# Kernel tuning notes

Hardware: AMD Instinct MI355X
Metric: run time of the kernel (lower is better)

Reference implementation:

```python
import jax, jax.numpy as jnp
import numpy as np

D_MODEL = 256
N_LEVELS = 4
N_HEADS = 4
N_POINTS = 8
D_FFN = 1024
SHAPES = [(100, 152), (50, 76), (25, 38), (13, 19)]  # (H, W) per level
BATCH = 2


def setup_inputs() -> dict:
    key = jax.random.key(0)
    ks = list(jax.random.split(key, 16))
    Len = sum(h * w for h, w in SHAPES)  # 20197
    s = 0.02

    def lin(k, fin, fout):
        k1, k2 = jax.random.split(k)
        return (jax.random.normal(k1, (fin, fout), jnp.float32) * s,
                jax.random.normal(k2, (fout,), jnp.float32) * s)

    W_off, b_off = lin(ks[0], D_MODEL, N_HEADS * N_LEVELS * N_POINTS * 2)
    W_attn, b_attn = lin(ks[1], D_MODEL, N_HEADS * N_LEVELS * N_POINTS)
    W_val, b_val = lin(ks[2], D_MODEL, D_MODEL)
    W_out, b_out = lin(ks[3], D_MODEL, D_MODEL)
    W1, b1 = lin(ks[4], D_MODEL, D_FFN)
    W2, b2 = lin(ks[5], D_FFN, D_MODEL)
    starts = np.concatenate([[0], np.cumsum([h * w for h, w in SHAPES])[:-1]])
    return {
        "src_feat": jax.random.normal(ks[6], (BATCH, Len, D_MODEL), jnp.float32),
        "reference_points": jax.random.uniform(ks[7], (BATCH, Len, N_LEVELS, 2), jnp.float32),
        "key_feat": jax.random.normal(ks[8], (BATCH, Len, D_MODEL), jnp.float32),
        "spatial_shapes": jnp.array(SHAPES, jnp.int32),
        "level_start_index": jnp.array(starts, jnp.int32),
        "W_off": W_off, "b_off": b_off, "W_attn": W_attn, "b_attn": b_attn,
        "W_val": W_val, "b_val": b_val, "W_out": W_out, "b_out": b_out,
        "W1": W1, "b1": b1, "W2": W2, "b2": b2,
        "g1": jnp.ones((D_MODEL,), jnp.float32), "be1": jnp.zeros((D_MODEL,), jnp.float32),
        "g2": jnp.ones((D_MODEL,), jnp.float32), "be2": jnp.zeros((D_MODEL,), jnp.float32),
    }


def _layernorm(x, g, b, eps=1e-5):
    mu = jnp.mean(x, -1, keepdims=True)
    var = jnp.mean(jnp.square(x - mu), -1, keepdims=True)
    return (x - mu) * jax.lax.rsqrt(var + eps) * g + b


def _bilinear(v, loc, H, W):
    # v: (N, M, H*W, D); loc: (N, M, Lq, P, 2) normalized [0,1]
    # Matches F.grid_sample(mode='bilinear', padding_mode='zeros', align_corners=False)
    x = loc[..., 0] * W - 0.5
    y = loc[..., 1] * H - 0.5
    x0 = jnp.floor(x)
    y0 = jnp.floor(y)
    wx = x - x0
    wy = y - y0
    N, M, Lq, P = x.shape
    out = None
    for dy in (0, 1):
        for dx in (0, 1):
            xi = x0 + dx
            yi = y0 + dy
            w = (wx if dx else 1.0 - wx) * (wy if dy else 1.0 - wy)
            valid = (xi >= 0) & (xi < W) & (yi >= 0) & (yi < H)
            idx = (jnp.clip(yi, 0, H - 1) * W + jnp.clip(xi, 0, W - 1)).astype(jnp.int32)
            g = jnp.take_along_axis(v, idx.reshape(N, M, Lq * P, 1), axis=2)
            g = g.reshape(N, M, Lq, P, -1) * (w * jnp.asarray(valid, v.dtype))[..., None]
            out = g if out is None else out + g
    return out  # (N, M, Lq, P, D)


def reference(src_feat, reference_points, key_feat, spatial_shapes, level_start_index,
              W_off, b_off, W_attn, b_attn, W_val, b_val, W_out, b_out,
              W1, b1, W2, b2, g1, be1, g2, be2):
    N, Lq, C = src_feat.shape
    M, L, P = N_HEADS, N_LEVELS, N_POINTS
    D = C // M
    shapes = np.asarray(spatial_shapes)  # static per-level (H, W)
    # --- MSDeformAttn ---
    value = (key_feat @ W_val + b_val).reshape(N, -1, M, D)
    off = (src_feat @ W_off + b_off).reshape(N, Lq, M, L, P, 2)
    attn = jax.nn.softmax((src_feat @ W_attn + b_attn).reshape(N, Lq, M, L * P), axis=-1)
    attn = attn.reshape(N, Lq, M, L, P)
    normalizer = jnp.stack([spatial_shapes[:, 1], spatial_shapes[:, 0]], -1).astype(src_feat.dtype)  # (L,2)=(W,H)
    loc = reference_points[:, :, None, :, None, :] + off / normalizer[None, None, None, :, None, :]
    out = jnp.zeros((N, M, Lq, D), src_feat.dtype)
    start = 0
    for l in range(L):
        H, W = int(shapes[l, 0]), int(shapes[l, 1])
        v = value[:, start:start + H * W].transpose(0, 2, 1, 3)  # (N,M,HW,D)
        samp = _bilinear(v, loc[:, :, :, l].transpose(0, 2, 1, 3, 4), H, W)  # (N,M,Lq,P,D)
        out = out + jnp.einsum('nmqpd,nqmp->nmqd', samp, attn[:, :, :, l])
        start += H * W
    out = out.transpose(0, 2, 1, 3).reshape(N, Lq, C)
    src2 = out @ W_out + b_out
    # --- residual + norm + FFN (light=False, dropout=0) ---
    x = _layernorm(src_feat + src2, g1, be1)
    ffn = jax.nn.relu(x @ W1 + b1) @ W2 + b2
    x = _layernorm(x + ffn, g2, be2)
    return (x, loc, attn)
```

## Files before the change

kernel.cpp:

```cpp
#include <hip/hip_runtime.h>
#include <hip/hip_bf16.h>

#define LQ 20197
#define NBATCH 2
#define MROWS 40394
#define MR256 ((size_t)MROWS * 256)

typedef __attribute__((ext_vector_type(8))) short bf16x8;
typedef __attribute__((ext_vector_type(4))) float f32x4;
typedef __attribute__((ext_vector_type(2))) float f32x2;

__device__ __forceinline__ unsigned short f2bf(float f) {
    unsigned u = __float_as_uint(f);
    return (unsigned short)((u + 0x7fff + ((u >> 16) & 1)) >> 16);
}
__device__ __forceinline__ float bf2f(unsigned short b) {
    return __uint_as_float((unsigned)b << 16);
}

__global__ __launch_bounds__(256) void prep_w_k(
    const float* __restrict__ Wv, const float* __restrict__ Wo,
    const float* __restrict__ Wa, const float* __restrict__ Wu,
    const float* __restrict__ W1, const float* __restrict__ W2,
    const float* __restrict__ ba,
    unsigned short* __restrict__ BTv, unsigned short* __restrict__ BTo,
    unsigned short* __restrict__ BTa, unsigned short* __restrict__ BTu,
    unsigned short* __restrict__ BT1, unsigned short* __restrict__ BT2,
    float* __restrict__ battn)
{
    const size_t id0 = (size_t)blockIdx.x * blockDim.x + threadIdx.x;
    const size_t stride = (size_t)gridDim.x * blockDim.x;
    for (size_t i = id0; i < 65536; i += stride) {
        const int n = (int)(i >> 8), k = (int)(i & 255);
        BTv[i] = f2bf(Wv[k * 256 + n]);
        BTo[i] = f2bf(Wo[k * 256 + n]);
        BTu[i] = f2bf(Wu[k * 256 + n]);
        BTa[i] = (n < 128) ? f2bf(Wa[k * 128 + n]) : (unsigned short)0;
    }
    for (size_t i = id0; i < 262144; i += stride) {
        const int n = (int)(i >> 8), k = (int)(i & 255);
        BT1[i] = f2bf(W1[(size_t)k * 1024 + n]);
        const int n2 = (int)(i >> 10), k2 = (int)(i & 1023);
        BT2[i] = f2bf(W2[(size_t)k2 * 256 + n2]);
    }
    if (id0 < 256) battn[id0] = (id0 < 128) ? ba[id0] : 0.f;
}

enum { EP_VAL = 0, EP_LOC = 1, EP_ATTN = 2, EP_LN = 3, EP_FFN1 = 4 };

template<int EP, bool AF32>
__global__ __launch_bounds__(256) void gemm_k(
    const void* __restrict__ Ap, const unsigned short* __restrict__ BT,
    const float* __restrict__ bias, const float* __restrict__ aux,
    const float* __restrict__ g, const float* __restrict__ be,
    void* outp, void* outp2)
{
    __shared__ __align__(16) unsigned short As[64 * 64];
    __shared__ __align__(16) unsigned short Bs[256 * 64];
    __shared__ float ps[64][4], pq[64][4];
    __shared__ float mu_s[64], rs_s[64];

    const int tid = threadIdx.x;
    const int l = tid & 63, w = tid >> 6;
    const int lc = l & 15, rg = l >> 4;
    const int rowBase = blockIdx.x * 64;
    const unsigned short* BTb = BT + (size_t)blockIdx.y * 65536;

    f32x4 acc[4][4] = {};

    for (int k0 = 0; k0 < 256; k0 += 64) {
        if (k0) __syncthreads();
        #pragma unroll
        for (int p = 0; p < 2; ++p) {
            const int idx = tid + p * 256;
            const int r = idx >> 3, s = idx & 7;
            const int row = rowBase + r;
            bf16x8 v = {};
            if (AF32) {
                if (row < MROWS) {
                    const float* A = (const float*)Ap;
                    const float4 v0 = *(const float4*)(A + (size_t)row * 256 + k0 + s * 8);
                    const float4 v1 = *(const float4*)(A + (size_t)row * 256 + k0 + s * 8 + 4);
                    v[0] = (short)f2bf(v0.x); v[1] = (short)f2bf(v0.y);
                    v[2] = (short)f2bf(v0.z); v[3] = (short)f2bf(v0.w);
                    v[4] = (short)f2bf(v1.x); v[5] = (short)f2bf(v1.y);
                    v[6] = (short)f2bf(v1.z); v[7] = (short)f2bf(v1.w);
                }
            } else {
                if (row < MROWS)
                    v = *(const bf16x8*)((const unsigned short*)Ap + (size_t)row * 256 + k0 + s * 8);
            }
            *(bf16x8*)&As[r * 64 + ((s ^ (r & 7)) << 3)] = v;
        }
        #pragma unroll
        for (int p = 0; p < 8; ++p) {
            const int idx = tid + p * 256;
            const int n = idx >> 3, s = idx & 7;
            bf16x8 v = *(const bf16x8*)(BTb + (size_t)n * 256 + k0 + s * 8);
            *(bf16x8*)&Bs[n * 64 + ((s ^ (n & 7)) << 3)] = v;
        }
        __syncthreads();
        #pragma unroll
        for (int kk = 0; kk < 2; ++kk) {
            bf16x8 aF[4], bF[4];
            const int sl = kk * 4 + rg;
            #pragma unroll
            for (int i = 0; i < 4; ++i) {
                const int r = i * 16 + lc;
                aF[i] = *(const bf16x8*)&As[r * 64 + ((sl ^ (r & 7)) << 3)];
            }
            #pragma unroll
            for (int j = 0; j < 4; ++j) {
                const int n = w * 64 + j * 16 + lc;
                bF[j] = *(const bf16x8*)&Bs[n * 64 + ((sl ^ (n & 7)) << 3)];
            }
            #pragma unroll
            for (int i = 0; i < 4; ++i)
                #pragma unroll
                for (int j = 0; j < 4; ++j)
                    acc[i][j] = __builtin_amdgcn_mfma_f32_16x16x32_bf16(aF[i], bF[j], acc[i][j], 0, 0, 0);
        }
    }

    if (EP == EP_VAL) {
        unsigned short* out = (unsigned short*)outp;
        #pragma unroll
        for (int i = 0; i < 4; ++i)
            #pragma unroll
            for (int r4 = 0; r4 < 4; ++r4) {
                const int row = rowBase + i * 16 + rg * 4 + r4;
                if (row >= MROWS) continue;
                #pragma unroll
                for (int j = 0; j < 4; ++j) {
                    const int col = w * 64 + j * 16 + lc;
                    out[(size_t)row * 256 + col] = f2bf(acc[i][j][r4] + bias[col]);
                }
            }
    } else if (EP == EP_FFN1) {
        unsigned short* h0 = (unsigned short*)outp;
        unsigned short* h1 = (unsigned short*)outp2;
        unsigned short* hb = (blockIdx.y < 2) ? h0 : h1;
        const int cbase = (blockIdx.y & 1) * 256;
        #pragma unroll
        for (int i = 0; i < 4; ++i)
            #pragma unroll
            for (int r4 = 0; r4 < 4; ++r4) {
                const int row = rowBase + i * 16 + rg * 4 + r4;
                if (row >= MROWS) continue;
                #pragma unroll
                for (int j = 0; j < 4; ++j) {
                    const int col = w * 64 + j * 16 + lc;
                    const float t = fmaxf(acc[i][j][r4] + bias[blockIdx.y * 256 + col], 0.f);
                    hb[(size_t)row * 512 + cbase + col] = f2bf(t);
                }
            }
    } else if (EP == EP_LOC) {
        float* out = (float*)outp;
        const float INV[8] = {1.f/152, 1.f/100, 1.f/76, 1.f/50, 1.f/38, 1.f/25, 1.f/19, 1.f/13};
        #pragma unroll
        for (int i = 0; i < 4; ++i)
            #pragma unroll
            for (int r4 = 0; r4 < 4; ++r4) {
                const int row = rowBase + i * 16 + rg * 4 + r4;
                if (row >= MROWS) continue;
                #pragma unroll
                for (int j = 0; j < 4; ++j) {
                    const int col = w * 64 + j * 16 + lc;
                    const int lvl = (col >> 4) & 3, xy = col & 1;
                    const float off = acc[i][j][r4] + bias[col];
                    const float ref = aux[(size_t)row * 8 + lvl * 2 + xy];
                    out[(size_t)row * 256 + col] = ref + off * INV[lvl * 2 + xy];
                }
            }
    } else if (EP == EP_ATTN) {
        if (w >= 2) return;
        float* out = (float*)outp;
        #pragma unroll
        for (int i = 0; i < 4; ++i)
            #pragma unroll
            for (int r4 = 0; r4 < 4; ++r4) {
                const int row = rowBase + i * 16 + rg * 4 + r4;
                float v[4];
                #pragma unroll
                for (int j = 0; j < 4; ++j) v[j] = acc[i][j][r4] + bias[w * 64 + j * 16 + lc];
                float mA = fmaxf(v[0], v[1]), mB = fmaxf(v[2], v[3]);
                #pragma unroll
                for (int o = 1; o <= 8; o <<= 1) {
                    mA = fmaxf(mA, __shfl_xor(mA, o));
                    mB = fmaxf(mB, __shfl_xor(mB, o));
                }
                float e[4];
                e[0] = __expf(v[0] - mA); e[1] = __expf(v[1] - mA);
                e[2] = __expf(v[2] - mB); e[3] = __expf(v[3] - mB);
                float sA = e[0] + e[1], sB = e[2] + e[3];
                #pragma unroll
                for (int o = 1; o <= 8; o <<= 1) {
                    sA += __shfl_xor(sA, o);
                    sB += __shfl_xor(sB, o);
                }
                if (row >= MROWS) continue;
                #pragma unroll
                for (int j = 0; j < 4; ++j) {
                    const int col = w * 64 + j * 16 + lc;
                    out[(size_t)row * 128 + col] = e[j] / (j < 2 ? sA : sB);
                }
            }
    } else {
        unsigned short* out = (unsigned short*)outp;
        #pragma unroll
        for (int i = 0; i < 4; ++i)
            #pragma unroll
            for (int r4 = 0; r4 < 4; ++r4) {
                const int row = rowBase + i * 16 + rg * 4 + r4;
                float s = 0.f, q = 0.f;
                #pragma unroll
                for (int j = 0; j < 4; ++j) {
                    const int col = w * 64 + j * 16 + lc;
                    float t = acc[i][j][r4] + bias[col];
                    if (row < MROWS) t += aux[(size_t)row * 256 + col];
                    acc[i][j][r4] = t;
                    s += t; q += t * t;
                }
                #pragma unroll
                for (int o = 1; o <= 8; o <<= 1) { s += __shfl_xor(s, o); q += __shfl_xor(q, o); }
                if (lc == 0) { ps[i * 16 + rg * 4 + r4][w] = s; pq[i * 16 + rg * 4 + r4][w] = q; }
            }
        __syncthreads();
        if (tid < 64) {
            const float s = ps[tid][0] + ps[tid][1] + ps[tid][2] + ps[tid][3];
            const float q = pq[tid][0] + pq[tid][1] + pq[tid][2] + pq[tid][3];
            const float m = s * (1.f / 256.f);
            mu_s[tid] = m;
            rs_s[tid] = rsqrtf(q * (1.f / 256.f) - m * m + 1e-5f);
        }
        __syncthreads();
        #pragma unroll
        for (int i = 0; i < 4; ++i)
            #pragma unroll
            for (int r4 = 0; r4 < 4; ++r4) {
                const int rl = i * 16 + rg * 4 + r4;
                const int row = rowBase + rl;
                if (row >= MROWS) continue;
                const float m = mu_s[rl], r = rs_s[rl];
                #pragma unroll
                for (int j = 0; j < 4; ++j) {
                    const int col = w * 64 + j * 16 + lc;
                    out[(size_t)row * 256 + col] = f2bf((acc[i][j][r4] - m) * r * g[col] + be[col]);
                }
            }
    }
}

__global__ __launch_bounds__(256) void ffn2_k(
    const unsigned short* __restrict__ h0, const unsigned short* __restrict__ h1,
    const unsigned short* __restrict__ BT2,
    const float* __restrict__ bias, const unsigned short* __restrict__ xb,
    const float* __restrict__ g, const float* __restrict__ be,
    float* __restrict__ out)
{
    __shared__ __align__(16) unsigned short As[64 * 64];
    __shared__ __align__(16) unsigned short Bs[256 * 64];
    __shared__ float ps[64][4], pq[64][4];
    __shared__ float mu_s[64], rs_s[64];

    const int tid = threadIdx.x;
    const int l = tid & 63, w = tid >> 6;
    const int lc = l & 15, rg = l >> 4;
    const int rowBase = blockIdx.x * 64;

    f32x4 acc[4][4] = {};

    for (int kc = 0; kc < 16; ++kc) {
        if (kc) __syncthreads();
        const unsigned short* Ab = (kc < 8) ? h0 : h1;
        const int koff = (kc & 7) * 64;
        #pragma unroll
        for (int p = 0; p < 2; ++p) {
            const int idx = tid + p * 256;
            const int r = idx >> 3, s = idx & 7;
            const int row = rowBase + r;
            bf16x8 v = {};
            if (row < MROWS) v = *(const bf16x8*)(Ab + (size_t)row * 512 + koff + s * 8);
            *(bf16x8*)&As[r * 64 + ((s ^ (r & 7)) << 3)] = v;
        }
        #pragma unroll
        for (int p = 0; p < 8; ++p) {
            const int idx = tid + p * 256;
            const int n = idx >> 3, s = idx & 7;
            bf16x8 v = *(const bf16x8*)(BT2 + (size_t)n * 1024 + kc * 64 + s * 8);
            *(bf16x8*)&Bs[n * 64 + ((s ^ (n & 7)) << 3)] = v;
        }
        __syncthreads();
        #pragma unroll
        for (int kk = 0; kk < 2; ++kk) {
            bf16x8 aF[4], bF[4];
            const int sl = kk * 4 + rg;
            #pragma unroll
            for (int i = 0; i < 4; ++i) {
                const int r = i * 16 + lc;
                aF[i] = *(const bf16x8*)&As[r * 64 + ((sl ^ (r & 7)) << 3)];
            }
            #pragma unroll
            for (int j = 0; j < 4; ++j) {
                const int n = w * 64 + j * 16 + lc;
                bF[j] = *(const bf16x8*)&Bs[n * 64 + ((sl ^ (n & 7)) << 3)];
            }
            #pragma unroll
            for (int i = 0; i < 4; ++i)
                #pragma unroll
                for (int j = 0; j < 4; ++j)
                    acc[i][j] = __builtin_amdgcn_mfma_f32_16x16x32_bf16(aF[i], bF[j], acc[i][j], 0, 0, 0);
        }
    }

    #pragma unroll
    for (int i = 0; i < 4; ++i)
        #pragma unroll
        for (int r4 = 0; r4 < 4; ++r4) {
            const int row = rowBase + i * 16 + rg * 4 + r4;
            float s = 0.f, q = 0.f;
            #pragma unroll
            for (int j = 0; j < 4; ++j) {
                const int col = w * 64 + j * 16 + lc;
                float t = acc[i][j][r4] + bias[col];
                if (row < MROWS) t += bf2f(xb[(size_t)row * 256 + col]);
                acc[i][j][r4] = t;
                s += t; q += t * t;
            }
            #pragma unroll
            for (int o = 1; o <= 8; o <<= 1) { s += __shfl_xor(s, o); q += __shfl_xor(q, o); }
            if (lc == 0) { ps[i * 16 + rg * 4 + r4][w] = s; pq[i * 16 + rg * 4 + r4][w] = q; }
        }
    __syncthreads();
    if (tid < 64) {
        const float s = ps[tid][0] + ps[tid][1] + ps[tid][2] + ps[tid][3];
        const float q = pq[tid][0] + pq[tid][1] + pq[tid][2] + pq[tid][3];
        const float m = s * (1.f / 256.f);
        mu_s[tid] = m;
        rs_s[tid] = rsqrtf(q * (1.f / 256.f) - m * m + 1e-5f);
    }
    __syncthreads();
    #pragma unroll
    for (int i = 0; i < 4; ++i)
        #pragma unroll
        for (int r4 = 0; r4 < 4; ++r4) {
            const int rl = i * 16 + rg * 4 + r4;
            const int row = rowBase + rl;
            if (row >= MROWS) continue;
            const float m = mu_s[rl], r = rs_s[rl];
            #pragma unroll
            for (int j = 0; j < 4; ++j) {
                const int col = w * 64 + j * 16 + lc;
                out[(size_t)row * 256 + col] = (acc[i][j][r4] - m) * r * g[col] + be[col];
            }
        }
}

#define QB2 8
__global__ __launch_bounds__(256) void sample_k(
    const unsigned short* __restrict__ value, const float* __restrict__ loc_i,
    const float* __restrict__ attn_i, unsigned short* __restrict__ samp_o)
{
    constexpr int LVL_H[4] = {100, 50, 25, 13};
    constexpr int LVL_W[4] = {152, 76, 38, 19};
    constexpr int LVL_S[4] = {0, 15200, 19000, 19950};
    const int tid = threadIdx.x;

    const int nwg = gridDim.x;
    const int bid = blockIdx.x;
    const int xcd = bid & 7, lid = bid >> 3;
    const int qq = nwg >> 3, rr = nwg & 7;
    const int sw = (xcd < rr ? xcd * (qq + 1) : rr * (qq + 1) + (xcd - rr) * qq) + lid;
    const int rowBase = sw * QB2;

    __shared__ int2 sT[QB2][4][128];

    #pragma unroll
    for (int it = 0; it < 4; ++it) {
        const int item = tid + it * 256;
        const int qs = item >> 7;
        const int t  = item & 127;
        const int row = rowBase + qs;
        if (row < MROWS) {
            const int lv = (t >> 3) & 3;
            const int n = (row >= LQ) ? 1 : 0;
            const int H = LVL_H[lv], W = LVL_W[lv];
            const float lx = loc_i[(size_t)row * 256 + t * 2 + 0];
            const float ly = loc_i[(size_t)row * 256 + t * 2 + 1];
            const float a  = attn_i[(size_t)row * 128 + t];
            const float x = lx * (float)W - 0.5f;
            const float y = ly * (float)H - 0.5f;
            const float x0f = floorf(x), y0f = floorf(y);
            const float wx = x - x0f, wy = y - y0f;
            const int x0 = (int)x0f, y0 = (int)y0f;
            const int base = n * LQ + LVL_S[lv];
            #pragma unroll
            for (int nb = 0; nb < 4; ++nb) {
                const int dx = nb & 1, dy = nb >> 1;
                const int xi = x0 + dx, yi = y0 + dy;
                const bool valid = (xi >= 0) & (xi < W) & (yi >= 0) & (yi < H);
                const float wgt = (dx ? wx : 1.f - wx) * (dy ? wy : 1.f - wy) * a;
                const int xc = min(max(xi, 0), W - 1);
                const int yc = min(max(yi, 0), H - 1);
                const int off = (base + yc * W + xc) << 9;
                sT[qs][nb][t] = make_int2(off, valid ? __float_as_int(wgt) : 0);
            }
        }
    }
    __syncthreads();

    const int qs = tid >> 5;
    const int c8 = tid & 31;
    const int row = rowBase + qs;
    if (row >= MROWS) return;
    const int m = c8 >> 3;
    const char* vb = (const char*)value + c8 * 16;
    const int2* tp = &sT[qs][0][m * 32];

    f32x2 a0 = {0.f, 0.f}, a1 = {0.f, 0.f}, a2 = {0.f, 0.f}, a3 = {0.f, 0.f};
    #pragma unroll 4
    for (int i = 0; i < 128; ++i) {
        const int t0 = i >> 2, nb = i & 3;
        const int2 ow = tp[nb * 128 + t0];
        const float w = __int_as_float(ow.y);
        const uint4 u = *(const uint4*)(vb + ow.x);
        const f32x2 wv = {w, w};
        f32x2 p;
        p.x = __uint_as_float(u.x << 16); p.y = __uint_as_float(u.x & 0xffff0000u);
        a0 = __builtin_elementwise_fma(p, wv, a0);
        p.x = __uint_as_float(u.y << 16); p.y = __uint_as_float(u.y & 0xffff0000u);
        a1 = __builtin_elementwise_fma(p, wv, a1);
        p.x = __uint_as_float(u.z << 16); p.y = __uint_as_float(u.z & 0xffff0000u);
        a2 = __builtin_elementwise_fma(p, wv, a2);
        p.x = __uint_as_float(u.w << 16); p.y = __uint_as_float(u.w & 0xffff0000u);
        a3 = __builtin_elementwise_fma(p, wv, a3);
    }
    uint4 o;
    o.x = (unsigned)f2bf(a0.x) | ((unsigned)f2bf(a0.y) << 16);
    o.y = (unsigned)f2bf(a1.x) | ((unsigned)f2bf(a1.y) << 16);
    o.z = (unsigned)f2bf(a2.x) | ((unsigned)f2bf(a2.y) << 16);
    o.w = (unsigned)f2bf(a3.x) | ((unsigned)f2bf(a3.y) << 16);
    *(uint4*)(samp_o + (size_t)row * 256 + c8 * 8) = o;
}

extern "C" void kernel_launch(void* const* d_in, const int* in_sizes, int n_in,
                              void* d_out, int out_size, void* d_ws, size_t ws_size,
                              hipStream_t stream)
{
    const float* src_feat = (const float*)d_in[0];
    const float* refpts   = (const float*)d_in[1];
    const float* key_feat = (const float*)d_in[2];
    const float* W_off  = (const float*)d_in[5];
    const float* b_off  = (const float*)d_in[6];
    const float* W_attn = (const float*)d_in[7];
    const float* b_attn = (const float*)d_in[8];
    const float* W_val  = (const float*)d_in[9];
    const float* b_val  = (const float*)d_in[10];
    const float* W_out  = (const float*)d_in[11];
    const float* b_out  = (const float*)d_in[12];
    const float* W1  = (const float*)d_in[13];
    const float* b1  = (const float*)d_in[14];
    const float* W2  = (const float*)d_in[15];
    const float* b2  = (const float*)d_in[16];
    const float* g1  = (const float*)d_in[17];
    const float* be1 = (const float*)d_in[18];
    const float* g2  = (const float*)d_in[19];
    const float* be2 = (const float*)d_in[20];

    float* out = (float*)d_out;
    float* x_out    = out;
    float* loc_out  = out + MR256;
    float* attn_out = out + 2 * MR256;

    char* ws = (char*)d_ws;
    unsigned short* BTv   = (unsigned short*)(ws + 0);
    unsigned short* BTo   = (unsigned short*)(ws + 131072);
    unsigned short* BTa   = (unsigned short*)(ws + 262144);
    unsigned short* BTu   = (unsigned short*)(ws + 393216);
    unsigned short* BT1   = (unsigned short*)(ws + 524288);
    unsigned short* BT2   = (unsigned short*)(ws + 1048576);
    float*          battn = (float*)(ws + 1572864);
    unsigned short* value = (unsigned short*)(ws + 2097152);
    unsigned short* samp  = (unsigned short*)(ws + 2097152 + MR256 * 2);
    unsigned short* xb    = (unsigned short*)(ws + 2097152 + MR256 * 4);
    unsigned short* h0    = value;
    unsigned short* h1    = (unsigned short*)x_out;

    const int RB = (MROWS + 63) / 64;

    prep_w_k<<<512, 256, 0, stream>>>(W_val, W_off, W_attn, W_out, W1, W2, b_attn,
                                      BTv, BTo, BTa, BTu, BT1, BT2, battn);
    gemm_k<EP_VAL, true><<<dim3(RB, 1), 256, 0, stream>>>(key_feat, BTv, b_val, nullptr, nullptr, nullptr, value, nullptr);
    gemm_k<EP_LOC, true><<<dim3(RB, 1), 256, 0, stream>>>(src_feat, BTo, b_off, refpts, nullptr, nullptr, loc_out, nullptr);
    gemm_k<EP_ATTN, true><<<dim3(RB, 1), 256, 0, stream>>>(src_feat, BTa, battn, nullptr, nullptr, nullptr, attn_out, nullptr);
    sample_k<<<(MROWS + QB2 - 1) / QB2, 256, 0, stream>>>(value, loc_out, attn_out, samp);
    gemm_k<EP_LN, false><<<dim3(RB, 1), 256, 0, stream>>>(samp, BTu, b_out, src_feat, g1, be1, xb, nullptr);
    gemm_k<EP_FFN1, false><<<dim3(RB, 4), 256, 0, stream>>>(xb, BT1, b1, nullptr, nullptr, nullptr, h0, h1);
    ffn2_k<<<dim3(RB, 1), 256, 0, stream>>>(h0, h1, BT2, b2, xb, g2, be2, x_out);
}
```

Before: 345.5 us.

## Use direct global-to-LDS loads with pre-swizzled weight and activation layouts

The GEMM kernels now fill shared memory with global_load_lds (direct global-to-LDS DMA) instead of routing data through registers. To keep the XOR bank swizzle, the weights are pre-swizzled during preparation, and the bf16 intermediate activations (LN output, FFN hidden, sampled features) are written in swizzled order by the producing kernels. The sampling kernel's shared table is padded to reduce bank conflicts. In exchange, the layout contract between kernels gets more complex, and partial tail tiles still use the register path.

```diff
diff --git a/kernel.cpp b/kernel.cpp
--- a/kernel.cpp
+++ b/kernel.cpp
@@ -16,6 +16,16 @@
 }
 __device__ __forceinline__ float bf2f(unsigned short b) {
     return __uint_as_float((unsigned)b << 16);
+}
+
+__device__ __forceinline__ void gload16(const void* g, void* l) {
+    __builtin_amdgcn_global_load_lds(
+        (const __attribute__((address_space(1))) unsigned int*)g,
+        (__attribute__((address_space(3))) unsigned int*)l, 16, 0, 0);
+}
+
+__device__ __forceinline__ int swz_k(int n, int kk) {
+    return (kk & ~63) | (((((kk >> 3) & 7) ^ (n & 7))) << 3) | (kk & 7);
 }
 
 __global__ __launch_bounds__(256) void prep_w_k(
@@ -31,17 +41,18 @@
     const size_t id0 = (size_t)blockIdx.x * blockDim.x + threadIdx.x;
     const size_t stride = (size_t)gridDim.x * blockDim.x;
     for (size_t i = id0; i < 65536; i += stride) {
-        const int n = (int)(i >> 8), k = (int)(i & 255);
+        const int n = (int)(i >> 8), kk = (int)(i & 255);
+        const int k = swz_k(n, kk);
         BTv[i] = f2bf(Wv[k * 256 + n]);
         BTo[i] = f2bf(Wo[k * 256 + n]);
         BTu[i] = f2bf(Wu[k * 256 + n]);
         BTa[i] = (n < 128) ? f2bf(Wa[k * 128 + n]) : (unsigned short)0;
     }
     for (size_t i = id0; i < 262144; i += stride) {
-        const int n = (int)(i >> 8), k = (int)(i & 255);
-        BT1[i] = f2bf(W1[(size_t)k * 1024 + n]);
-        const int n2 = (int)(i >> 10), k2 = (int)(i & 1023);
-        BT2[i] = f2bf(W2[(size_t)k2 * 256 + n2]);
+        const int n = (int)(i >> 8), kk = (int)(i & 255);
+        BT1[i] = f2bf(W1[(size_t)swz_k(n, kk) * 1024 + n]);
+        const int n2 = (int)(i >> 10), kk2 = (int)(i & 1023);
+        BT2[i] = f2bf(W2[(size_t)swz_k(n2, kk2) * 256 + n2]);
     }
     if (id0 < 256) battn[id0] = (id0 < 128) ? ba[id0] : 0.f;
 }
@@ -64,21 +75,29 @@
     const int l = tid & 63, w = tid >> 6;
     const int lc = l & 15, rg = l >> 4;
     const int rowBase = blockIdx.x * 64;
+    const int wb = tid & ~63;
     const unsigned short* BTb = BT + (size_t)blockIdx.y * 65536;
+    const bool fullA = (rowBase + 64 <= MROWS);
 
     f32x4 acc[4][4] = {};
 
     for (int k0 = 0; k0 < 256; k0 += 64) {
         if (k0) __syncthreads();
         #pragma unroll
-        for (int p = 0; p < 2; ++p) {
+        for (int p = 0; p < 8; ++p) {
             const int idx = tid + p * 256;
-            const int r = idx >> 3, s = idx & 7;
-            const int row = rowBase + r;
-            bf16x8 v = {};
-            if (AF32) {
+            gload16(BTb + (size_t)(idx >> 3) * 256 + k0 + (idx & 7) * 8,
+                    &Bs[(p * 256 + wb) * 8]);
+        }
+        if (AF32) {
+            const float* A = (const float*)Ap;
+            #pragma unroll
+            for (int p = 0; p < 2; ++p) {
+                const int idx = tid + p * 256;
+                const int r = idx >> 3, s = idx & 7;
+                const int row = rowBase + r;
+                bf16x8 v = {};
                 if (row < MROWS) {
-                    const float* A = (const float*)Ap;
                     const float4 v0 = *(const float4*)(A + (size_t)row * 256 + k0 + s * 8);
                     const float4 v1 = *(const float4*)(A + (size_t)row * 256 + k0 + s * 8 + 4);
                     v[0] = (short)f2bf(v0.x); v[1] = (short)f2bf(v0.y);
@@ -86,18 +105,26 @@
                     v[4] = (short)f2bf(v1.x); v[5] = (short)f2bf(v1.y);
                     v[6] = (short)f2bf(v1.z); v[7] = (short)f2bf(v1.w);
                 }
-            } else {
+                *(bf16x8*)&As[r * 64 + ((s ^ (r & 7)) << 3)] = v;
+            }
+        } else if (fullA) {
+            #pragma unroll
+            for (int p = 0; p < 2; ++p) {
+                const int idx = tid + p * 256;
+                gload16((const unsigned short*)Ap + (size_t)(rowBase + (idx >> 3)) * 256 + k0 + (idx & 7) * 8,
+                        &As[(p * 256 + wb) * 8]);
+            }
+        } else {
+            #pragma unroll
+            for (int p = 0; p < 2; ++p) {
+                const int idx = tid + p * 256;
+                const int r = idx >> 3, s = idx & 7;
+                const int row = rowBase + r;
+                bf16x8 v = {};
                 if (row < MROWS)
                     v = *(const bf16x8*)((const unsigned short*)Ap + (size_t)row * 256 + k0 + s * 8);
-            }
-            *(bf16x8*)&As[r * 64 + ((s ^ (r & 7)) << 3)] = v;
-        }
-        #pragma unroll
-        for (int p = 0; p < 8; ++p) {
-            const int idx = tid + p * 256;
-            const int n = idx >> 3, s = idx & 7;
-            bf16x8 v = *(const bf16x8*)(BTb + (size_t)n * 256 + k0 + s * 8);
-            *(bf16x8*)&Bs[n * 64 + ((s ^ (n & 7)) << 3)] = v;
+                *(bf16x8*)&As[idx * 8] = v;
+            }
         }
         __syncthreads();
         #pragma unroll
@@ -139,8 +166,6 @@
     } else if (EP == EP_FFN1) {
         unsigned short* h0 = (unsigned short*)outp;
         unsigned short* h1 = (unsigned short*)outp2;
-        unsigned short* hb = (blockIdx.y < 2) ? h0 : h1;
-        const int cbase = (blockIdx.y & 1) * 256;
         #pragma unroll
         for (int i = 0; i < 4; ++i)
             #pragma unroll
@@ -149,9 +174,13 @@
                 if (row >= MROWS) continue;
                 #pragma unroll
                 for (int j = 0; j < 4; ++j) {
-                    const int col = w * 64 + j * 16 + lc;
-                    const float t = fmaxf(acc[i][j][r4] + bias[blockIdx.y * 256 + col], 0.f);
-                    hb[(size_t)row * 512 + cbase + col] = f2bf(t);
+                    const int colg = blockIdx.y * 256 + w * 64 + j * 16 + lc;
+                    const float t = fmaxf(acc[i][j][r4] + bias[colg], 0.f);
+                    unsigned short* hb = (colg < 512) ? h0 : h1;
+                    const int lcol = colg & 511;
+                    const int gg = lcol >> 3, e = lcol & 7;
+                    const int gs = (gg & 56) | ((gg & 7) ^ (row & 7));
+                    hb[(size_t)row * 512 + gs * 8 + e] = f2bf(t);
                 }
             }
     } else if (EP == EP_LOC) {
@@ -245,7 +274,9 @@
                 #pragma unroll
                 for (int j = 0; j < 4; ++j) {
                     const int col = w * 64 + j * 16 + lc;
-                    out[(size_t)row * 256 + col] = f2bf((acc[i][j][r4] - m) * r * g[col] + be[col]);
+                    const int gg = col >> 3, e = col & 7;
+                    const int gs = (gg & 24) | ((gg & 7) ^ (row & 7));
+                    out[(size_t)row * 256 + gs * 8 + e] = f2bf((acc[i][j][r4] - m) * r * g[col] + be[col]);
                 }
             }
     }
@@ -267,28 +298,38 @@
     const int l = tid & 63, w = tid >> 6;
     const int lc = l & 15, rg = l >> 4;
     const int rowBase = blockIdx.x * 64;
+    const int wb = tid & ~63;
+    const bool fullA = (rowBase + 64 <= MROWS);
 
     f32x4 acc[4][4] = {};
 
     for (int kc = 0; kc < 16; ++kc) {
         if (kc) __syncthreads();
+        #pragma unroll
+        for (int p = 0; p < 8; ++p) {
+            const int idx = tid + p * 256;
+            gload16(BT2 + (size_t)(idx >> 3) * 1024 + kc * 64 + (idx & 7) * 8,
+                    &Bs[(p * 256 + wb) * 8]);
+        }
         const unsigned short* Ab = (kc < 8) ? h0 : h1;
         const int koff = (kc & 7) * 64;
-        #pragma unroll
-        for (int p = 0; p < 2; ++p) {
-            const int idx = tid + p * 256;
-            const int r = idx >> 3, s = idx & 7;
-            const int row = rowBase + r;
-            bf16x8 v = {};
-            if (row < MROWS) v = *(const bf16x8*)(Ab + (size_t)row * 512 + koff + s * 8);
-            *(bf16x8*)&As[r * 64 + ((s ^ (r & 7)) << 3)] = v;
-        }
-        #pragma unroll
-        for (int p = 0; p < 8; ++p) {
-            const int idx = tid + p * 256;
-            const int n = idx >> 3, s = idx & 7;
-            bf16x8 v = *(const bf16x8*)(BT2 + (size_t)n * 1024 + kc * 64 + s * 8);
-            *(bf16x8*)&Bs[n * 64 + ((s ^ (n & 7)) << 3)] = v;
+        if (fullA) {
+            #pragma unroll
+            for (int p = 0; p < 2; ++p) {
+                const int idx = tid + p * 256;
+                gload16(Ab + (size_t)(rowBase + (idx >> 3)) * 512 + koff + (idx & 7) * 8,
+                        &As[(p * 256 + wb) * 8]);
+            }
+        } else {
+            #pragma unroll
+            for (int p = 0; p < 2; ++p) {
+                const int idx = tid + p * 256;
+                const int r = idx >> 3, s = idx & 7;
+                const int row = rowBase + r;
+                bf16x8 v = {};
+                if (row < MROWS) v = *(const bf16x8*)(Ab + (size_t)row * 512 + koff + s * 8);
+                *(bf16x8*)&As[idx * 8] = v;
+            }
         }
         __syncthreads();
         #pragma unroll
@@ -323,7 +364,11 @@
             for (int j = 0; j < 4; ++j) {
                 const int col = w * 64 + j * 16 + lc;
                 float t = acc[i][j][r4] + bias[col];
-                if (row < MROWS) t += bf2f(xb[(size_t)row * 256 + col]);
+                if (row < MROWS) {
+                    const int gg = col >> 3, e = col & 7;
+                    const int gs = (gg & 24) | ((gg & 7) ^ (row & 7));
+                    t += bf2f(xb[(size_t)row * 256 + gs * 8 + e]);
+                }
                 acc[i][j][r4] = t;
                 s += t; q += t * t;
             }
@@ -373,7 +418,7 @@
     const int sw = (xcd < rr ? xcd * (qq + 1) : rr * (qq + 1) + (xcd - rr) * qq) + lid;
     const int rowBase = sw * QB2;
 
-    __shared__ int2 sT[QB2][4][128];
+    __shared__ int2 sT[QB2][4][132];
 
     #pragma unroll
     for (int it = 0; it < 4; ++it) {
@@ -394,6 +439,7 @@
             const float wx = x - x0f, wy = y - y0f;
             const int x0 = (int)x0f, y0 = (int)y0f;
             const int base = n * LQ + LVL_S[lv];
+            const int tp = (t >> 5) * 33 + (t & 31);
             #pragma unroll
             for (int nb = 0; nb < 4; ++nb) {
                 const int dx = nb & 1, dy = nb >> 1;
@@ -403,7 +449,7 @@
                 const int xc = min(max(xi, 0), W - 1);
                 const int yc = min(max(yi, 0), H - 1);
                 const int off = (base + yc * W + xc) << 9;
-                sT[qs][nb][t] = make_int2(off, valid ? __float_as_int(wgt) : 0);
+                sT[qs][nb][tp] = make_int2(off, valid ? __float_as_int(wgt) : 0);
             }
         }
     }
@@ -415,13 +461,13 @@
     if (row >= MROWS) return;
     const int m = c8 >> 3;
     const char* vb = (const char*)value + c8 * 16;
-    const int2* tp = &sT[qs][0][m * 32];
+    const int mb = m * 33;
 
     f32x2 a0 = {0.f, 0.f}, a1 = {0.f, 0.f}, a2 = {0.f, 0.f}, a3 = {0.f, 0.f};
     #pragma unroll 4
     for (int i = 0; i < 128; ++i) {
         const int t0 = i >> 2, nb = i & 3;
-        const int2 ow = tp[nb * 128 + t0];
+        const int2 ow = sT[qs][nb][mb + t0];
         const float w = __int_as_float(ow.y);
         const uint4 u = *(const uint4*)(vb + ow.x);
         const f32x2 wv = {w, w};
@@ -440,7 +486,8 @@
     o.y = (unsigned)f2bf(a1.x) | ((unsigned)f2bf(a1.y) << 16);
     o.z = (unsigned)f2bf(a2.x) | ((unsigned)f2bf(a2.y) << 16);
     o.w = (unsigned)f2bf(a3.x) | ((unsigned)f2bf(a3.y) << 16);
-    *(uint4*)(samp_o + (size_t)row * 256 + c8 * 8) = o;
+    const int slot = (c8 & 24) | ((c8 & 7) ^ (row & 7));
+    *(uint4*)(samp_o + (size_t)row * 256 + slot * 8) = o;
 }
 
 extern "C" void kernel_launch(void* const* d_in, const int* in_sizes, int n_in,
```

Result: no change. 346.8 us (+0.3%).
